# Performance work log

Hardware: AMD Instinct MI355X
Metric: run time of the kernel (lower is better)

The kernel has to match this reference:

```python
import jax, jax.numpy as jnp
import numpy as np

D_MODEL = 1024
M = 4
NUM_EXPERTS = 8
TOP_K = 2
B, T = 2, 2048


def setup_inputs() -> dict:
    key = jax.random.key(0)
    ks = jax.random.split(key, 4)
    d_ff = D_MODEL * M
    x = jax.random.normal(ks[0], (B, T, D_MODEL), dtype=jnp.float32)
    # torch nn.Linear(d_model, num_experts, bias=False): stored here as (D, E) so logits = x @ gate_w
    gate_w = jax.random.normal(ks[1], (D_MODEL, NUM_EXPERTS), dtype=jnp.float32) * 0.02
    w1 = jax.random.normal(ks[2], (NUM_EXPERTS, D_MODEL, d_ff), dtype=jnp.float32) * 0.02
    b1 = jnp.zeros((NUM_EXPERTS, d_ff), dtype=jnp.float32)
    w2 = jax.random.normal(ks[3], (NUM_EXPERTS, d_ff, D_MODEL), dtype=jnp.float32) * 0.02
    b2 = jnp.zeros((NUM_EXPERTS, D_MODEL), dtype=jnp.float32)
    return {"x": x, "gate_w": gate_w, "w1": w1, "b1": b1, "w2": w2, "b2": b2}


def reference(x, gate_w, w1, b1, w2, b2):
    Bb, Tt, D = x.shape
    E = w1.shape[0]
    N = Bb * Tt
    # gating: top-k logits -> softmax over the k selected experts
    logits = jnp.einsum('btd,de->bte', x, gate_w)               # (B,T,E)
    top_v, top_i = jax.lax.top_k(logits, TOP_K)                 # (B,T,K)
    top_w = jax.nn.softmax(top_v, axis=-1)                      # (B,T,K)

    xf = x.reshape(N, D)
    idx = top_i.reshape(N, TOP_K)
    wts = top_w.reshape(N, TOP_K)
    # dense combine weights: comb[n, e] = sum_k wts[n,k] * [idx[n,k]==e]
    comb = jnp.zeros((N, E), dtype=x.dtype).at[jnp.arange(N)[:, None], idx].add(wts)

    # per-expert dense 2-layer MLP (exact erf GELU, matching torch F.gelu default),
    # combined with gate weights (zero weight == token not routed to expert).
    out = jnp.zeros((N, D), dtype=x.dtype)
    for e in range(E):
        h = jax.nn.gelu(xf @ w1[e] + b1[e], approximate=False)  # (N, D*M)
        out = out + comb[:, e:e + 1] * (h @ w2[e] + b2[e])      # (N, D)
    return out.reshape(Bb, Tt, D)
```

## Files before the change

kernel.cpp:

```cpp
#include <hip/hip_runtime.h>
#include <hip/hip_bf16.h>
#include <math.h>

#define D_MODEL 1024
#define D_FF    4096
#define NEXP    8
#define NTOK    4096
#define NROUTED 8192
#define MAXJOBS 40

typedef __attribute__((ext_vector_type(8))) short bf16x8;
typedef __attribute__((ext_vector_type(4))) float f32x4;
typedef __attribute__((ext_vector_type(4))) unsigned short us4;

#define WS_CNT   0
#define WS_CNT2  64
#define WS_OFF   128
#define WS_JOBS  192
#define WS_TI    512
#define WS_TW    (WS_TI + NTOK*2*4)
#define WS_TOK   (WS_TW + NTOK*2*4)
#define WS_GWT   (WS_TOK + NROUTED*4)
#define WS_XG    (((WS_GWT + NROUTED*4) + 255) & ~255)
#define WS_H     (WS_XG + (size_t)NROUTED*D_MODEL*2)
#define WS_WT    (WS_H + (size_t)NROUTED*D_FF*2)

__device__ __forceinline__ unsigned short f2bf(float f){
  union { float f; unsigned u; } a; a.f = f;
  unsigned u = a.u;
  u = u + 0x7FFF + ((u >> 16) & 1);
  return (unsigned short)(u >> 16);
}

__device__ __forceinline__ void gload_lds16(const void* g, void* l){
  __builtin_amdgcn_global_load_lds((const __attribute__((address_space(1))) void*)g,
                                   (__attribute__((address_space(3))) void*)l, 16, 0, 0);
}

__global__ void moe_gate_kernel(const float* __restrict__ x, const float* __restrict__ gw,
                                int* cnt, int* __restrict__ ti, float* __restrict__ tw){
  int n = blockIdx.x*4 + (threadIdx.x >> 6);
  int lane = threadIdx.x & 63;
  const float* xr = x + (size_t)n * D_MODEL;
  float acc[NEXP];
  #pragma unroll
  for (int e=0;e<NEXP;e++) acc[e] = 0.f;
  for (int d=lane; d<D_MODEL; d+=64){
    float xv = xr[d];
    #pragma unroll
    for (int e=0;e<NEXP;e++) acc[e] += xv * gw[d*NEXP + e];
  }
  #pragma unroll
  for (int e=0;e<NEXP;e++){
    #pragma unroll
    for (int o=32;o;o>>=1) acc[e] += __shfl_down(acc[e], o, 64);
  }
  if (lane == 0){
    int i0 = 0; float v0 = acc[0];
    #pragma unroll
    for (int e=1;e<NEXP;e++) if (acc[e] > v0){ v0 = acc[e]; i0 = e; }
    int i1 = -1; float v1 = -1e30f;
    #pragma unroll
    for (int e=0;e<NEXP;e++) if (e != i0 && acc[e] > v1){ v1 = acc[e]; i1 = e; }
    float p = expf(v1 - v0);
    float inv = 1.f / (1.f + p);
    ti[n*2] = i0; ti[n*2+1] = i1;
    tw[n*2] = inv; tw[n*2+1] = p * inv;
    atomicAdd(&cnt[i0], 1); atomicAdd(&cnt[i1], 1);
  }
}

__global__ void moe_prefix_kernel(const int* __restrict__ cnt, int* __restrict__ off,
                                  int* __restrict__ jobs){
  if (threadIdx.x == 0){
    int s = 0;
    for (int e=0;e<NEXP;e++){ off[e] = s; s += cnt[e]; }
    off[NEXP] = s;
    int idx = 0;
    for (int e=0;e<NEXP;e++){
      int ns = (cnt[e] + 255) >> 8;
      for (int q=0;q<ns;q++) jobs[1+idx++] = (e<<16) | q;
    }
    jobs[0] = idx;
  }
}

__global__ void moe_assign_kernel(const float* __restrict__ x, const int* __restrict__ ti,
                                  const float* __restrict__ tw, const int* __restrict__ off,
                                  int* cnt2, int* __restrict__ tok, float* __restrict__ gwt,
                                  unsigned short* __restrict__ Xg){
  __shared__ int ss[2];
  int n = blockIdx.x;
  if (threadIdx.x == 0){
    int i0 = ti[n*2], i1 = ti[n*2+1];
    int s0 = off[i0] + atomicAdd(&cnt2[i0], 1);
    int s1 = off[i1] + atomicAdd(&cnt2[i1], 1);
    tok[s0] = n; tok[s1] = n;
    gwt[s0] = tw[n*2]; gwt[s1] = tw[n*2+1];
    ss[0] = s0; ss[1] = s1;
  }
  __syncthreads();
  int s0 = ss[0], s1 = ss[1];
  int t = threadIdx.x;
  f32x4 v = *(const f32x4*)(x + (size_t)n * D_MODEL + t*4);
  us4 pk = { f2bf(v.x), f2bf(v.y), f2bf(v.z), f2bf(v.w) };
  __builtin_nontemporal_store(pk, (us4*)(Xg + (size_t)s0 * D_MODEL + t*4));
  __builtin_nontemporal_store(pk, (us4*)(Xg + (size_t)s1 * D_MODEL + t*4));
}

__global__ __launch_bounds__(256) void transpose_bf16_kernel(
    const float* __restrict__ W, unsigned short* __restrict__ Wt, int K, int F){
  __shared__ float tile[64][65];
  int e = blockIdx.z;
  int f0 = blockIdx.x * 64, k0 = blockIdx.y * 64;
  const float* Wb = W + (size_t)e * K * F;
  unsigned short* Wtb = Wt + (size_t)e * F * K;
  int tid = threadIdx.x;
  #pragma unroll
  for (int i=0;i<4;i++){
    int idx = i*256 + tid;
    int r = idx >> 4, c4 = (idx & 15) * 4;
    f32x4 v = __builtin_nontemporal_load((const f32x4*)(Wb + (size_t)(k0 + r) * F + f0 + c4));
    tile[r][c4] = v.x; tile[r][c4+1] = v.y; tile[r][c4+2] = v.z; tile[r][c4+3] = v.w;
  }
  __syncthreads();
  #pragma unroll
  for (int i=0;i<4;i++){
    int idx = i*256 + tid;
    int f = idx >> 4, k4 = (idx & 15) * 4;
    us4 pk = { f2bf(tile[k4][f]), f2bf(tile[k4+1][f]), f2bf(tile[k4+2][f]), f2bf(tile[k4+3][f]) };
    __builtin_nontemporal_store(pk, (us4*)(Wtb + (size_t)(f0 + f) * K + k0 + k4));
  }
}

template<int MODE>
__global__ __launch_bounds__(1024) void moe_gemm_kernel(
    char* __restrict__ wsb, const unsigned short* __restrict__ Bt,
    const float* __restrict__ bias, float* __restrict__ out)
{
  const int* jobs = (const int*)(wsb + WS_JOBS);
  if ((int)blockIdx.y >= jobs[0]) return;
  const int jb = jobs[1 + blockIdx.y];
  const int e = jb >> 16;
  const int row0 = (jb & 0xffff) << 8;

  const int* off = (const int*)(wsb + WS_OFF);
  const int n0 = off[e];
  const int ne = off[e+1] - n0;

  constexpr int K  = (MODE==1) ? D_MODEL : D_FF;
  constexpr int NT = (MODE==1) ? 32 : 64;
  const int bx     = (MODE==1) ? blockIdx.x : (blockIdx.x & 3);
  const int kchunk = (MODE==1) ? 0 : (blockIdx.x >> 2);
  const int n_off  = bx * 256;
  const size_t kcb = (size_t)kchunk * 4096;

  const unsigned short* Ag  = (const unsigned short*)(wsb + (MODE==1 ? (size_t)WS_XG : (size_t)WS_H));
  const unsigned short* Bgt = Bt + (size_t)e * D_FF * D_MODEL;

  __shared__ __align__(16) char lds[3*32768];

  const int tid = threadIdx.x, lane = tid & 63, w = tid >> 6;
  const int wr = w >> 2, wc = w & 3;

  const int rA   = w*16 + (lane >> 2);
  const int qs   = ((lane & 3) ^ ((rA >> 1) & 3)) << 4;
  int grA = row0 + rA; if (grA >= ne) grA = ne - 1;
  const char* aSrc = (const char*)(Ag + (size_t)(n0 + grA) * K) + kcb + qs;
  const char* bSrc = (const char*)(Bgt + (size_t)(n_off + rA) * K) + kcb + qs;
  const int dA = w*1024, dB = 16384 + w*1024;

  const int q0 = lane >> 4;
  int aoff[4], boff[4];
  #pragma unroll
  for (int mi=0; mi<4; mi++){
    int row = wr*64 + mi*16 + (lane & 15);
    aoff[mi] = row*64 + ((q0 ^ ((row>>1)&3)) << 4);
  }
  #pragma unroll
  for (int ni=0; ni<4; ni++){
    int col = wc*64 + ni*16 + (lane & 15);
    boff[ni] = 16384 + col*64 + ((q0 ^ ((col>>1)&3)) << 4);
  }

  f32x4 acc[4][4];
  #pragma unroll
  for (int i=0;i<4;i++)
    #pragma unroll
    for (int j=0;j<4;j++) acc[i][j] = (f32x4){0.f,0.f,0.f,0.f};

  #define STAGE(tt, ss) { \
    gload_lds16(aSrc + (size_t)(tt)*64, lds + (ss)*32768 + dA); \
    gload_lds16(bSrc + (size_t)(tt)*64, lds + (ss)*32768 + dB); }

  STAGE(0, 0);
  STAGE(1, 1);

  for (int t = 0; t < NT; ++t){
    if (t < NT-1) asm volatile("s_waitcnt vmcnt(2)" ::: "memory");
    else          asm volatile("s_waitcnt vmcnt(0)" ::: "memory");
    __builtin_amdgcn_s_barrier();
    __builtin_amdgcn_sched_barrier(0);

    if (t + 2 < NT) STAGE(t + 2, (t + 2) % 3);

    const char* base = lds + (t % 3) * 32768;
    bf16x8 a[4], b[4];
    #pragma unroll
    for (int mi=0; mi<4; mi++) a[mi] = *(const bf16x8*)(base + aoff[mi]);
    #pragma unroll
    for (int ni=0; ni<4; ni++) b[ni] = *(const bf16x8*)(base + boff[ni]);

    asm volatile("s_waitcnt lgkmcnt(0)" ::: "memory");
    __builtin_amdgcn_sched_barrier(0);
    __builtin_amdgcn_s_setprio(1);
    #pragma unroll
    for (int ni=0; ni<4; ni++)
      #pragma unroll
      for (int mi=0; mi<4; mi++)
        acc[mi][ni] = __builtin_amdgcn_mfma_f32_16x16x32_bf16(a[mi], b[ni], acc[mi][ni], 0, 0, 0);
    __builtin_amdgcn_s_setprio(0);
    __builtin_amdgcn_sched_barrier(0);
  }
  #undef STAGE

  if (MODE == 1){
    const float* b1 = bias + (size_t)e * D_FF;
    unsigned short* H = (unsigned short*)(wsb + (size_t)WS_H);
    #pragma unroll
    for (int mi=0; mi<4; mi++){
      int rbase = wr*64 + mi*16 + ((lane>>4)<<2);
      #pragma unroll
      for (int rr=0;rr<4;rr++){
        int lrow = rbase + rr;
        if (row0 + lrow < ne){
          size_t hb = (size_t)(n0 + row0 + lrow) * D_FF;
          #pragma unroll
          for (int ni=0; ni<4; ni++){
            int gcol = n_off + wc*64 + ni*16 + (lane&15);
            float v = acc[mi][ni][rr] + b1[gcol];
            v = 0.5f * v * (1.f + erff(v * 0.70710678118654752f));
            __builtin_nontemporal_store(f2bf(v), H + hb + gcol);
          }
        }
      }
    }
  } else {
    const float* b2 = bias + (size_t)e * D_MODEL;
    const int* tok = (const int*)(wsb + WS_TOK);
    const float* gwt = (const float*)(wsb + WS_GWT);
    #pragma unroll
    for (int mi=0; mi<4; mi++){
      int rbase = wr*64 + mi*16 + ((lane>>4)<<2);
      #pragma unroll
      for (int rr=0;rr<4;rr++){
        int lrow = rbase + rr;
        if (row0 + lrow < ne){
          int slot = n0 + row0 + lrow;
          int tk = tok[slot];
          float g = gwt[slot];
          float* orow = out + (size_t)tk * D_MODEL;
          #pragma unroll
          for (int ni=0; ni<4; ni++){
            int gcol = n_off + wc*64 + ni*16 + (lane&15);
            float bb = (kchunk == 0) ? b2[gcol] : 0.f;
            atomicAdd(orow + gcol, (acc[mi][ni][rr] + bb) * g);
          }
        }
      }
    }
  }
}

extern "C" void kernel_launch(void* const* d_in, const int* in_sizes, int n_in,
                              void* d_out, int out_size, void* d_ws, size_t ws_size,
                              hipStream_t stream){
  const float* x   = (const float*)d_in[0];
  const float* gw  = (const float*)d_in[1];
  const float* w1  = (const float*)d_in[2];
  const float* b1  = (const float*)d_in[3];
  const float* w2  = (const float*)d_in[4];
  const float* b2  = (const float*)d_in[5];
  float* out = (float*)d_out;
  char* ws = (char*)d_ws;
  unsigned short* Wt = (unsigned short*)(ws + (size_t)WS_WT);

  hipMemsetAsync(ws, 0, 512, stream);
  hipMemsetAsync(out, 0, (size_t)NTOK * D_MODEL * sizeof(float), stream);

  moe_gate_kernel<<<NTOK/4, 256, 0, stream>>>(x, gw, (int*)(ws+WS_CNT),
                                              (int*)(ws+WS_TI), (float*)(ws+WS_TW));
  moe_prefix_kernel<<<1, 64, 0, stream>>>((const int*)(ws+WS_CNT), (int*)(ws+WS_OFF),
                                          (int*)(ws+WS_JOBS));
  moe_assign_kernel<<<NTOK, 256, 0, stream>>>(x, (const int*)(ws+WS_TI),
                                              (const float*)(ws+WS_TW), (const int*)(ws+WS_OFF),
                                              (int*)(ws+WS_CNT2), (int*)(ws+WS_TOK),
                                              (float*)(ws+WS_GWT),
                                              (unsigned short*)(ws + (size_t)WS_XG));
  transpose_bf16_kernel<<<dim3(D_FF/64, D_MODEL/64, NEXP), 256, 0, stream>>>(w1, Wt, D_MODEL, D_FF);
  moe_gemm_kernel<1><<<dim3(D_FF/256, MAXJOBS), 1024, 0, stream>>>(ws, Wt, b1, out);
  transpose_bf16_kernel<<<dim3(D_MODEL/64, D_FF/64, NEXP), 256, 0, stream>>>(w2, Wt, D_FF, D_MODEL);
  moe_gemm_kernel<2><<<dim3((D_MODEL/256)*2, MAXJOBS), 1024, 0, stream>>>(ws, Wt, b2, out);
}
```

Measured before the change: 570.8 us.

## Halve GEMM block to 512 threads with 128x64 warp tiles and register double-buffering

The grouped MoE GEMM drops from 1024 to 512 threads per block while keeping the 256x256 output tile. Each wave now computes a 128x64 sub-tile (8x4 MFMA accumulators), so it reuses more operands per LDS read and issues twice as many global-to-LDS loads per stage. The main loop is unrolled by two, and LDS fragments for the next k-step are read into a second register set while the current step's MFMAs run, to overlap LDS latency with compute. Launch bounds (512,2) allow two blocks per CU, but the larger accumulator and fragment footprint raises register pressure and could cause spills.

```diff
diff --git a/kernel.cpp b/kernel.cpp
--- a/kernel.cpp
+++ b/kernel.cpp
@@ -134,7 +134,7 @@
 }
 
 template<int MODE>
-__global__ __launch_bounds__(1024) void moe_gemm_kernel(
+__global__ __launch_bounds__(512, 2) void moe_gemm_kernel(
     char* __restrict__ wsb, const unsigned short* __restrict__ Bt,
     const float* __restrict__ bias, float* __restrict__ out)
 {
@@ -163,18 +163,21 @@
   const int tid = threadIdx.x, lane = tid & 63, w = tid >> 6;
   const int wr = w >> 2, wc = w & 3;
 
-  const int rA   = w*16 + (lane >> 2);
-  const int qs   = ((lane & 3) ^ ((rA >> 1) & 3)) << 4;
-  int grA = row0 + rA; if (grA >= ne) grA = ne - 1;
-  const char* aSrc = (const char*)(Ag + (size_t)(n0 + grA) * K) + kcb + qs;
-  const char* bSrc = (const char*)(Bgt + (size_t)(n_off + rA) * K) + kcb + qs;
-  const int dA = w*1024, dB = 16384 + w*1024;
+  const int rs = w*16 + (lane >> 2);
+  const int qs = ((lane & 3) ^ ((rs >> 1) & 3)) << 4;
+  int gr0 = row0 + rs;        if (gr0 >= ne) gr0 = ne - 1;
+  int gr1 = row0 + 128 + rs;  if (gr1 >= ne) gr1 = ne - 1;
+  const char* aSrc0 = (const char*)(Ag + (size_t)(n0 + gr0) * K) + kcb + qs;
+  const char* aSrc1 = (const char*)(Ag + (size_t)(n0 + gr1) * K) + kcb + qs;
+  const char* bSrc0 = (const char*)(Bgt + (size_t)(n_off + rs) * K) + kcb + qs;
+  const char* bSrc1 = (const char*)(Bgt + (size_t)(n_off + 128 + rs) * K) + kcb + qs;
+  const int dstOff = w*1024;
 
   const int q0 = lane >> 4;
-  int aoff[4], boff[4];
-  #pragma unroll
-  for (int mi=0; mi<4; mi++){
-    int row = wr*64 + mi*16 + (lane & 15);
+  int aoff[8], boff[4];
+  #pragma unroll
+  for (int mi=0; mi<8; mi++){
+    int row = wr*128 + mi*16 + (lane & 15);
     aoff[mi] = row*64 + ((q0 ^ ((row>>1)&3)) << 4);
   }
   #pragma unroll
@@ -183,53 +186,75 @@
     boff[ni] = 16384 + col*64 + ((q0 ^ ((col>>1)&3)) << 4);
   }
 
-  f32x4 acc[4][4];
-  #pragma unroll
-  for (int i=0;i<4;i++)
+  f32x4 acc[8][4];
+  #pragma unroll
+  for (int i=0;i<8;i++)
     #pragma unroll
     for (int j=0;j<4;j++) acc[i][j] = (f32x4){0.f,0.f,0.f,0.f};
 
   #define STAGE(tt, ss) { \
-    gload_lds16(aSrc + (size_t)(tt)*64, lds + (ss)*32768 + dA); \
-    gload_lds16(bSrc + (size_t)(tt)*64, lds + (ss)*32768 + dB); }
+    size_t kb = (size_t)(tt)*64; \
+    char* d = lds + (ss)*32768; \
+    gload_lds16(aSrc0 + kb, d + dstOff); \
+    gload_lds16(aSrc1 + kb, d + 8192 + dstOff); \
+    gload_lds16(bSrc0 + kb, d + 16384 + dstOff); \
+    gload_lds16(bSrc1 + kb, d + 24576 + dstOff); }
+
+  #define READ(A_, B_, base_) { \
+    _Pragma("unroll") \
+    for (int mi=0; mi<8; mi++) A_[mi] = *(const bf16x8*)((base_) + aoff[mi]); \
+    _Pragma("unroll") \
+    for (int ni=0; ni<4; ni++) B_[ni] = *(const bf16x8*)((base_) + boff[ni]); }
+
+  #define MM(A_, B_) { \
+    __builtin_amdgcn_s_setprio(1); \
+    _Pragma("unroll") \
+    for (int ni=0; ni<4; ni++) \
+      _Pragma("unroll") \
+      for (int mi=0; mi<8; mi++) \
+        acc[mi][ni] = __builtin_amdgcn_mfma_f32_16x16x32_bf16(A_[mi], B_[ni], acc[mi][ni], 0, 0, 0); \
+    __builtin_amdgcn_s_setprio(0); }
+
+  bf16x8 aA[8], bA[4], aB[8], bB[4];
 
   STAGE(0, 0);
   STAGE(1, 1);
-
-  for (int t = 0; t < NT; ++t){
-    if (t < NT-1) asm volatile("s_waitcnt vmcnt(2)" ::: "memory");
-    else          asm volatile("s_waitcnt vmcnt(0)" ::: "memory");
+  asm volatile("s_waitcnt vmcnt(4)" ::: "memory");
+  __builtin_amdgcn_s_barrier();
+  READ(aA, bA, lds);
+
+  for (int t = 0; t < NT; t += 2){
+    if (t + 2 < NT){
+      STAGE(t + 2, (t + 2) % 3);
+      asm volatile("s_waitcnt vmcnt(4)" ::: "memory");
+    } else {
+      asm volatile("s_waitcnt vmcnt(0)" ::: "memory");
+    }
     __builtin_amdgcn_s_barrier();
-    __builtin_amdgcn_sched_barrier(0);
-
-    if (t + 2 < NT) STAGE(t + 2, (t + 2) % 3);
-
-    const char* base = lds + (t % 3) * 32768;
-    bf16x8 a[4], b[4];
-    #pragma unroll
-    for (int mi=0; mi<4; mi++) a[mi] = *(const bf16x8*)(base + aoff[mi]);
-    #pragma unroll
-    for (int ni=0; ni<4; ni++) b[ni] = *(const bf16x8*)(base + boff[ni]);
-
-    asm volatile("s_waitcnt lgkmcnt(0)" ::: "memory");
-    __builtin_amdgcn_sched_barrier(0);
-    __builtin_amdgcn_s_setprio(1);
-    #pragma unroll
-    for (int ni=0; ni<4; ni++)
-      #pragma unroll
-      for (int mi=0; mi<4; mi++)
-        acc[mi][ni] = __builtin_amdgcn_mfma_f32_16x16x32_bf16(a[mi], b[ni], acc[mi][ni], 0, 0, 0);
-    __builtin_amdgcn_s_setprio(0);
-    __builtin_amdgcn_sched_barrier(0);
+    READ(aB, bB, lds + ((t + 1) % 3) * 32768);
+    MM(aA, bA);
+    if (t + 2 < NT){
+      if (t + 3 < NT){
+        STAGE(t + 3, (t + 3) % 3);
+        asm volatile("s_waitcnt vmcnt(4)" ::: "memory");
+      } else {
+        asm volatile("s_waitcnt vmcnt(0)" ::: "memory");
+      }
+      __builtin_amdgcn_s_barrier();
+      READ(aA, bA, lds + ((t + 2) % 3) * 32768);
+    }
+    MM(aB, bB);
   }
   #undef STAGE
+  #undef READ
+  #undef MM
 
   if (MODE == 1){
     const float* b1 = bias + (size_t)e * D_FF;
     unsigned short* H = (unsigned short*)(wsb + (size_t)WS_H);
     #pragma unroll
-    for (int mi=0; mi<4; mi++){
-      int rbase = wr*64 + mi*16 + ((lane>>4)<<2);
+    for (int mi=0; mi<8; mi++){
+      int rbase = wr*128 + mi*16 + ((lane>>4)<<2);
       #pragma unroll
       for (int rr=0;rr<4;rr++){
         int lrow = rbase + rr;
@@ -250,8 +275,8 @@
     const int* tok = (const int*)(wsb + WS_TOK);
     const float* gwt = (const float*)(wsb + WS_GWT);
     #pragma unroll
-    for (int mi=0; mi<4; mi++){
-      int rbase = wr*64 + mi*16 + ((lane>>4)<<2);
+    for (int mi=0; mi<8; mi++){
+      int rbase = wr*128 + mi*16 + ((lane>>4)<<2);
       #pragma unroll
       for (int rr=0;rr<4;rr++){
         int lrow = rbase + rr;
@@ -298,7 +323,7 @@
                                               (float*)(ws+WS_GWT),
                                               (unsigned short*)(ws + (size_t)WS_XG));
   transpose_bf16_kernel<<<dim3(D_FF/64, D_MODEL/64, NEXP), 256, 0, stream>>>(w1, Wt, D_MODEL, D_FF);
-  moe_gemm_kernel<1><<<dim3(D_FF/256, MAXJOBS), 1024, 0, stream>>>(ws, Wt, b1, out);
+  moe_gemm_kernel<1><<<dim3(D_FF/256, MAXJOBS), 512, 0, stream>>>(ws, Wt, b1, out);
   transpose_bf16_kernel<<<dim3(D_MODEL/64, D_FF/64, NEXP), 256, 0, stream>>>(w2, Wt, D_FF, D_MODEL);
-  moe_gemm_kernel<2><<<dim3((D_MODEL/256)*2, MAXJOBS), 1024, 0, stream>>>(ws, Wt, b2, out);
-}
+  moe_gemm_kernel<2><<<dim3((D_MODEL/256)*2, MAXJOBS), 512, 0, stream>>>(ws, Wt, b2, out);
+}
```

After: 639.6 us. 1.12x slower.
